# Optimization experiments

Hardware: AMD Instinct MI355X
Metric: run time of the kernel (lower is better)

The kernel has to match this reference:

```python
import jax, jax.numpy as jnp
import numpy as np

B, F = 32, 8192
GRAVITY = 9.81007
GYRO_COV = 0.0032 ** 2   # per-axis gyroscope noise covariance
ACC_COV = 0.08 ** 2      # per-axis accelerometer noise covariance


def _skew(v):
    # v: (..., 3) -> (..., 3, 3) skew-symmetric (hat) matrix
    x, y, z = v[..., 0], v[..., 1], v[..., 2]
    o = jnp.zeros_like(x)
    return jnp.stack([
        jnp.stack([o, -z, y], -1),
        jnp.stack([z, o, -x], -1),
        jnp.stack([-y, x, o], -1)], -2)


def _qmul(a, b):
    # Hamilton product, xyzw convention (pypose layout): a (x) b
    ax, ay, az, aw = a[..., 0], a[..., 1], a[..., 2], a[..., 3]
    bx, by, bz, bw = b[..., 0], b[..., 1], b[..., 2], b[..., 3]
    return jnp.stack([
        aw * bx + ax * bw + ay * bz - az * by,
        aw * by - ax * bz + ay * bw + az * bx,
        aw * bz + ax * by - ay * bx + az * bw,
        aw * bw - ax * bx - ay * by - az * bz], -1)


def _so3_exp_quat(phi):
    # so3 exponential map -> unit quaternion (xyzw), numerically safe near 0
    th2 = jnp.sum(phi * phi, -1, keepdims=True)
    small = th2 < 1e-8
    th = jnp.sqrt(jnp.where(small, 1.0, th2))
    s = jnp.where(small, 0.5 - th2 / 48.0, jnp.sin(0.5 * th) / th)
    w = jnp.where(small, 1.0 - th2 / 8.0, jnp.cos(0.5 * th))
    return jnp.concatenate([phi * s, w], -1)


def _quat_to_mat(q):
    # unit quaternion (xyzw) -> rotation matrix (..., 3, 3)
    x, y, z, w = q[..., 0], q[..., 1], q[..., 2], q[..., 3]
    r0 = jnp.stack([1 - 2 * (y * y + z * z), 2 * (x * y - z * w), 2 * (x * z + y * w)], -1)
    r1 = jnp.stack([2 * (x * y + z * w), 1 - 2 * (x * x + z * z), 2 * (y * z - x * w)], -1)
    r2 = jnp.stack([2 * (x * z - y * w), 2 * (y * z + x * w), 1 - 2 * (x * x + y * y)], -1)
    return jnp.stack([r0, r1, r2], -2)


def _so3_Jr(phi):
    # Right Jacobian of SO3: Jr = I - c1*K + c2*K^2, safe near 0
    th2 = jnp.sum(phi * phi, -1)[..., None, None]
    small = th2 < 1e-8
    th2s = jnp.where(small, 1.0, th2)
    th = jnp.sqrt(th2s)
    c1 = jnp.where(small, 0.5 - th2 / 24.0, (1.0 - jnp.cos(th)) / th2s)
    c2 = jnp.where(small, 1.0 / 6.0 - th2 / 120.0, (th - jnp.sin(th)) / (th2s * th))
    K = _skew(phi)
    I = jnp.eye(3, dtype=phi.dtype)
    return I - c1 * K + c2 * (K @ K)


def setup_inputs() -> dict:
    key = jax.random.key(0)
    k1, k2, k3 = jax.random.split(key, 3)
    dt = jax.random.uniform(k1, (B, F, 1), dtype=jnp.float32) * 0.004 + 0.001
    gyro = jax.random.normal(k2, (B, F, 3), dtype=jnp.float32)
    acc = jax.random.normal(k3, (B, F, 3), dtype=jnp.float32)
    pos0 = jnp.zeros((B, 3), dtype=jnp.float32)
    vel0 = jnp.zeros((B, 3), dtype=jnp.float32)
    return {"dt": dt, "gyro": gyro, "acc": acc, "pos0": pos0, "vel0": vel0}


def _preintegrate(dt, gyro, acc, pos0, vel0):
    dtype = acc.dtype
    g = jnp.array([0.0, 0.0, GRAVITY], dtype=dtype)
    I3 = jnp.eye(3, dtype=dtype)

    # --- rotation integration: dR_{k+1} = dR_k Exp(w_k dt_k) ---
    w = gyro * dt                                             # (B,F,3)
    dq = _so3_exp_quat(w)                                     # (B,F,4) per-step increments
    incre_q = jax.lax.associative_scan(_qmul, dq, axis=1)     # cumprod q0 (x) ... (x) qk
    R_incl = _quat_to_mat(incre_q)                            # (B,F,3,3) inclusive DeltaR_{ik+1}
    R_pre = jnp.concatenate(
        [jnp.broadcast_to(I3, (R_incl.shape[0], 1, 3, 3)), R_incl[:, :-1]], axis=1)  # DeltaR_{ik}

    # gravity removed in body frame: a_k = acc_k - R_k^{-1} g  (R^{-1} g = R^T g)
    a = acc - jnp.einsum('bfji,j->bfi', R_incl, g)            # (B,F,3)

    # --- velocity / position integration ---
    dv_step = jnp.einsum('bfij,bfj->bfi', R_pre, a) * dt      # DeltaR_{ik} a_k dt
    dvel = jnp.cumsum(dv_step, axis=1)                        # Delta v
    vel = vel0[:, None, :] + dvel
    dvel_prev = jnp.concatenate([jnp.zeros_like(dvel[:, :1]), dvel[:, :-1]], axis=1)
    dpos = jnp.cumsum(dvel_prev * dt + 0.5 * dv_step * dt, axis=1)
    pos = pos0[:, None, :] + dpos

    # --- covariance propagation: C' = A C A^T + Bg Cg Bg^T + Ba Ca Ba^T ---
    Bn, Fn = dt.shape[0], dt.shape[1]
    dRT = jnp.swapaxes(_quat_to_mat(dq), -1, -2)              # Exp(w dt)^T
    Ra = jnp.einsum('bfij,bfjk->bfik', R_pre, _skew(a))       # DeltaR (a^)
    dt1 = dt[..., None]                                       # (B,F,1,1)

    A = jnp.zeros((Bn, Fn, 9, 9), dtype=dtype)
    A = A.at[..., 0:3, 0:3].set(dRT)
    A = A.at[..., 3:6, 0:3].set(-Ra * dt1)
    A = A.at[..., 6:9, 0:3].set(-0.5 * Ra * dt1 * dt1)
    A = A.at[..., 3:6, 3:6].set(I3)
    A = A.at[..., 6:9, 6:9].set(I3)
    A = A.at[..., 6:9, 3:6].set(I3 * dt1)

    qg = jnp.full((3,), GYRO_COV, dtype=dtype)
    qa = jnp.full((3,), ACC_COV, dtype=dtype)
    Bg = _so3_Jr(w) * dt1                                     # (B,F,3,3)
    Bv = R_pre * dt1
    Bp = 0.5 * R_pre * dt1 * dt1
    Ngg = jnp.einsum('bfik,k,bfjk->bfij', Bg, qg, Bg)
    Nvv = jnp.einsum('bfik,k,bfjk->bfij', Bv, qa, Bv)
    Nvp = jnp.einsum('bfik,k,bfjk->bfij', Bv, qa, Bp)
    Npp = jnp.einsum('bfik,k,bfjk->bfij', Bp, qa, Bp)
    N = jnp.zeros((Bn, Fn, 9, 9), dtype=dtype)
    N = N.at[..., 0:3, 0:3].set(Ngg)
    N = N.at[..., 3:6, 3:6].set(Nvv)
    N = N.at[..., 3:6, 6:9].set(Nvp)
    N = N.at[..., 6:9, 3:6].set(jnp.swapaxes(Nvp, -1, -2))
    N = N.at[..., 6:9, 6:9].set(Npp)

    def step(C, AN):
        Ak, Nk = AN
        C = jnp.einsum('bij,bjk,blk->bil', Ak, C, Ak) + Nk
        return C, None

    C0 = jnp.zeros((Bn, 9, 9), dtype=dtype)
    cov, _ = jax.lax.scan(step, C0, (jnp.moveaxis(A, 1, 0), jnp.moveaxis(N, 1, 0)))

    # init rot is identity -> output rot equals the incremental cumprod
    return incre_q, vel, pos, cov


def reference(dt, gyro, acc, pos0, vel0):
    return _preintegrate(dt, gyro, acc, pos0, vel0)
```

## Files before the change

kernel.cpp:

```cpp
#include <hip/hip_runtime.h>


#define BB 32
#define FF 8192
#define NCH 128
#define SLOT 61
#define GRAV 9.81007f
#define GCOV (0.0032f*0.0032f)
#define ACOV (0.08f*0.08f)

#define COV_OFF  0
#define VPRE_OFF 249856
#define QTOT_OFF 282624
#define QPRE_OFF 299008
#define VP_OFF   315392

struct Quat { float x, y, z, w; };

__device__ __forceinline__ Quat qmul(const Quat a, const Quat b) {
    Quat r;
    r.x = a.w*b.x + a.x*b.w + a.y*b.z - a.z*b.y;
    r.y = a.w*b.y - a.x*b.z + a.y*b.w + a.z*b.x;
    r.z = a.w*b.z + a.x*b.y - a.y*b.x + a.z*b.w;
    r.w = a.w*b.w - a.x*b.x - a.y*b.y - a.z*b.z;
    return r;
}

__device__ __forceinline__ Quat qshfl_up(const Quat a, int s) {
    Quat r;
    r.x=__shfl_up(a.x,s); r.y=__shfl_up(a.y,s);
    r.z=__shfl_up(a.z,s); r.w=__shfl_up(a.w,s);
    return r;
}

__device__ __forceinline__ Quat qexp3(float px, float py, float pz) {
    float th2 = px*px + py*py + pz*pz;
    float s, w;
    if (th2 < 1e-8f) {
        s = 0.5f - th2 * (1.0f/48.0f);
        w = 1.0f - th2 * 0.125f;
    } else {
        float th = sqrtf(th2);
        s = sinf(0.5f*th) / th;
        w = cosf(0.5f*th);
    }
    Quat q; q.x=px*s; q.y=py*s; q.z=pz*s; q.w=w; return q;
}

__device__ __forceinline__ void quat2mat(const Quat q, float* R) {
    float x=q.x, y=q.y, z=q.z, w=q.w;
    R[0]=1.0f-2.0f*(y*y+z*z); R[1]=2.0f*(x*y-z*w);       R[2]=2.0f*(x*z+y*w);
    R[3]=2.0f*(x*y+z*w);      R[4]=1.0f-2.0f*(x*x+z*z);  R[5]=2.0f*(y*z-x*w);
    R[6]=2.0f*(x*z-y*w);      R[7]=2.0f*(y*z+x*w);       R[8]=1.0f-2.0f*(x*x+y*y);
}

__device__ __forceinline__ void mm_nn(const float* A, const float* B, float* C) {
#pragma unroll
    for (int i=0;i<3;i++)
#pragma unroll
    for (int j=0;j<3;j++)
        C[3*i+j] = A[3*i+0]*B[0+j] + A[3*i+1]*B[3+j] + A[3*i+2]*B[6+j];
}

__device__ __forceinline__ void mm_nt(const float* A, const float* B, float* C) {
#pragma unroll
    for (int i=0;i<3;i++)
#pragma unroll
    for (int j=0;j<3;j++)
        C[3*i+j] = A[3*i+0]*B[3*j+0] + A[3*i+1]*B[3*j+1] + A[3*i+2]*B[3*j+2];
}

__device__ __forceinline__ void mm_tn(const float* A, const float* B, float* C) {
#pragma unroll
    for (int i=0;i<3;i++)
#pragma unroll
    for (int j=0;j<3;j++)
        C[3*i+j] = A[0+i]*B[0+j] + A[3+i]*B[3+j] + A[6+i]*B[6+j];
}

__device__ __forceinline__ void mm_nt_sym(const float* A, const float* B, float* O6) {
    O6[0]=A[0]*B[0]+A[1]*B[1]+A[2]*B[2];
    O6[1]=A[0]*B[3]+A[1]*B[4]+A[2]*B[5];
    O6[2]=A[0]*B[6]+A[1]*B[7]+A[2]*B[8];
    O6[3]=A[3]*B[3]+A[4]*B[4]+A[5]*B[5];
    O6[4]=A[3]*B[6]+A[4]*B[7]+A[5]*B[8];
    O6[5]=A[6]*B[6]+A[7]*B[7]+A[8]*B[8];
}

__device__ __forceinline__ void mm_nn_sym(const float* A, const float* B, float* O6) {
    O6[0]=A[0]*B[0]+A[1]*B[3]+A[2]*B[6];
    O6[1]=A[0]*B[1]+A[1]*B[4]+A[2]*B[7];
    O6[2]=A[0]*B[2]+A[1]*B[5]+A[2]*B[8];
    O6[3]=A[3]*B[1]+A[4]*B[4]+A[5]*B[7];
    O6[4]=A[3]*B[2]+A[4]*B[5]+A[5]*B[8];
    O6[5]=A[6]*B[2]+A[7]*B[5]+A[8]*B[8];
}

__device__ __forceinline__ void expand_sym(const float* t, float* M) {
    M[0]=t[0]; M[1]=t[1]; M[2]=t[2];
    M[3]=t[1]; M[4]=t[3]; M[5]=t[4];
    M[6]=t[2]; M[7]=t[4]; M[8]=t[5];
}

__device__ __forceinline__ void m_skew(const float* M, float v0, float v1, float v2, float* C) {
#pragma unroll
    for (int i=0;i<3;i++) {
        C[3*i+0] = M[3*i+1]*v2 - M[3*i+2]*v1;
        C[3*i+1] = M[3*i+2]*v0 - M[3*i+0]*v2;
        C[3*i+2] = M[3*i+0]*v1 - M[3*i+1]*v0;
    }
}

__device__ __forceinline__ void skew_m(float w0, float w1, float w2, const float* M, float* C) {
#pragma unroll
    for (int j=0;j<3;j++) {
        C[0+j] = -w2*M[3+j] + w1*M[6+j];
        C[3+j] =  w2*M[0+j] - w0*M[6+j];
        C[6+j] = -w1*M[0+j] + w0*M[3+j];
    }
}

__global__ __launch_bounds__(256) void k_chunktot(
    const float* __restrict__ dt, const float* __restrict__ gyro,
    float* __restrict__ qtot, float* __restrict__ outq)
{
    const int bid=blockIdx.x, b=bid>>5, wg=bid&31;
    const int tid=threadIdx.x, lane=tid&63, wid=tid>>6;
    const int c=wg*4+wid;
    const long k=(long)b*FF+(long)c*64+lane;
    float d=dt[k];
    Quat inc=qexp3(gyro[3*k+0]*d, gyro[3*k+1]*d, gyro[3*k+2]*d);
#pragma unroll
    for (int s=1;s<64;s<<=1) {
        Quat p=qshfl_up(inc,s);
        if (lane>=s) inc=qmul(p,inc);
    }
    { float4 o; o.x=inc.x; o.y=inc.y; o.z=inc.z; o.w=inc.w;
      reinterpret_cast<float4*>(outq)[k]=o; }
    if (lane==63) {
        float4 o; o.x=inc.x; o.y=inc.y; o.z=inc.z; o.w=inc.w;
        reinterpret_cast<float4*>(qtot)[b*NCH+c]=o;
    }
}

__global__ __launch_bounds__(128) void k_qpre(
    const float* __restrict__ qtot, float* __restrict__ qpre)
{
    const int b=blockIdx.x, c=threadIdx.x, lane=c&63, w=c>>6;
    __shared__ float4 w0t;
    __shared__ float4 all[NCH];
    float4 t=reinterpret_cast<const float4*>(qtot)[b*NCH+c];
    Quat inc; inc.x=t.x; inc.y=t.y; inc.z=t.z; inc.w=t.w;
#pragma unroll
    for (int s=1;s<64;s<<=1) {
        Quat p=qshfl_up(inc,s);
        if (lane>=s) inc=qmul(p,inc);
    }
    if (w==0 && lane==63) { float4 o; o.x=inc.x;o.y=inc.y;o.z=inc.z;o.w=inc.w; w0t=o; }
    __syncthreads();
    if (w==1) { Quat p; p.x=w0t.x;p.y=w0t.y;p.z=w0t.z;p.w=w0t.w; inc=qmul(p,inc); }
    { float4 o; o.x=inc.x;o.y=inc.y;o.z=inc.z;o.w=inc.w; all[c]=o; }
    __syncthreads();
    float4 pre;
    if (c==0) { pre.x=0.f;pre.y=0.f;pre.z=0.f;pre.w=1.f; }
    else pre=all[c-1];
    reinterpret_cast<float4*>(qpre)[b*NCH+c]=pre;
}

#define RSTR 66
__global__ __launch_bounds__(256) void k_main(
    const float* __restrict__ dt, const float* __restrict__ gyro,
    const float* __restrict__ acc, const float* __restrict__ qpre_g,
    float* __restrict__ outq, float* __restrict__ cov, float* __restrict__ vp_g,
    float* __restrict__ outv, float* __restrict__ outp)
{
    __shared__ float red[4][23][RSTR];
    const int bid=blockIdx.x, b=bid>>5, wg=bid&31;
    const int tid=threadIdx.x, lane=tid&63, wid=tid>>6;
    const int c=wg*4+wid;
    const long k=(long)b*FF+(long)c*64+lane;

    const float d=dt[k];
    const float wx=gyro[3*k+0]*d, wy=gyro[3*k+1]*d, wz=gyro[3*k+2]*d;

    Quat qloc;
    { float4 t=reinterpret_cast<const float4*>(outq)[k];
      qloc.x=t.x; qloc.y=t.y; qloc.z=t.z; qloc.w=t.w; }
    float4 tp=reinterpret_cast<const float4*>(qpre_g)[b*NCH+c];
    Quat qpre; qpre.x=tp.x; qpre.y=tp.y; qpre.z=tp.z; qpre.w=tp.w;
    Quat qi=qmul(qpre,qloc);
    { float4 o; o.x=qi.x;o.y=qi.y;o.z=qi.z;o.w=qi.w;
      reinterpret_cast<float4*>(outq)[k]=o; }

    Quat ql1=qshfl_up(qloc,1);
    if (lane==0) { ql1.x=0.f; ql1.y=0.f; ql1.z=0.f; ql1.w=1.f; }
    Quat cq; cq.x=-ql1.x; cq.y=-ql1.y; cq.z=-ql1.z; cq.w=ql1.w;
    Quat dqq=qmul(cq,qloc);

    float a0=acc[3*k+0]-GRAV*2.0f*(qi.x*qi.z-qi.y*qi.w);
    float a1=acc[3*k+1]-GRAV*2.0f*(qi.y*qi.z+qi.x*qi.w);
    float a2=acc[3*k+2]-GRAV*(1.0f-2.0f*(qi.x*qi.x+qi.y*qi.y));

    float Rl[9]; quat2mat(ql1,Rl);
    float b0=Rl[0]*a0+Rl[1]*a1+Rl[2]*a2;
    float b1=Rl[3]*a0+Rl[4]*a1+Rl[5]*a2;
    float b2=Rl[6]*a0+Rl[7]*a1+Rl[8]*a2;
    float m0=d*b0, m1=d*b1, m2=d*b2;

    float td=d, M0=m0, M1=m1, M2=m2;
#pragma unroll
    for (int s=1;s<64;s<<=1) {
        float p3=__shfl_up(td,s), p0=__shfl_up(M0,s), p1=__shfl_up(M1,s), p2=__shfl_up(M2,s);
        if (lane>=s) { td+=p3; M0+=p0; M1+=p1; M2+=p2; }
    }
    float Dtot=__shfl(td,63);
    float tau = Dtot - td;
    float cn = 0.5f*d + tau;
    float n0=cn*m0, n1=cn*m1, n2=cn*m2;
    float N0=n0, N1=n1, N2=n2;
#pragma unroll
    for (int s=1;s<64;s<<=1) {
        float p0=__shfl_up(N0,s),p1=__shfl_up(N1,s),p2=__shfl_up(N2,s);
        if (lane>=s){ N0+=p0; N1+=p1; N2+=p2; }
    }
    float u0=(M0-0.5f*m0)*d, u1=(M1-0.5f*m1)*d, u2=(M2-0.5f*m2)*d;
    float U0=u0, U1=u1, U2=u2;
#pragma unroll
    for (int s=1;s<64;s<<=1) {
        float p0=__shfl_up(U0,s),p1=__shfl_up(U1,s),p2=__shfl_up(U2,s);
        if (lane>=s){ U0+=p0; U1+=p1; U2+=p2; }
    }
    float Mt0=__shfl(M0,63), Mt1=__shfl(M1,63), Mt2=__shfl(M2,63);
    float Nt0=__shfl(N0,63), Nt1=__shfl(N1,63), Nt2=__shfl(N2,63);
    float mp0=Mt0-M0, mp1=Mt1-M1, mp2=Mt2-M2;
    float np0=Nt0-N0, np1=Nt1-N1, np2=Nt2-N2;

    float Rp9[9]; quat2mat(qpre,Rp9);
    float pv0=Rp9[0]*M0+Rp9[1]*M1+Rp9[2]*M2;
    float pv1=Rp9[3]*M0+Rp9[4]*M1+Rp9[5]*M2;
    float pv2=Rp9[6]*M0+Rp9[7]*M1+Rp9[8]*M2;
    float pp0=Rp9[0]*U0+Rp9[1]*U1+Rp9[2]*U2;
    float pp1=Rp9[3]*U0+Rp9[4]*U1+Rp9[5]*U2;
    float pp2=Rp9[6]*U0+Rp9[7]*U1+Rp9[8]*U2;
    outv[3*k+0]=pv0; outv[3*k+1]=pv1; outv[3*k+2]=pv2;
    outp[3*k+0]=pp0; outp[3*k+1]=pp1; outp[3*k+2]=pp2;

    const long wsbase=((long)b*NCH+c)*SLOT;
    if (lane==63) {
        float* vp=vp_g+(long)(b*NCH+c)*8;
        vp[0]=pv0; vp[1]=pv1; vp[2]=pv2;
        vp[3]=pp0; vp[4]=pp1; vp[5]=pp2;
        vp[6]=td;
        cov[wsbase+45]=qloc.x; cov[wsbase+46]=qloc.y; cov[wsbase+47]=qloc.z; cov[wsbase+48]=qloc.w;
        cov[wsbase+49]=qpre.x; cov[wsbase+50]=qpre.y; cov[wsbase+51]=qpre.z; cov[wsbase+52]=qpre.w;
        cov[wsbase+53]=M0; cov[wsbase+54]=M1; cov[wsbase+55]=M2;
        cov[wsbase+56]=N0; cov[wsbase+57]=N1; cov[wsbase+58]=N2;
        cov[wsbase+59]=td;
    }

    float th2 = wx*wx + wy*wy + wz*wz;
    float c1, c2;
    if (th2 < 1e-8f) { c1 = 0.5f - th2*(1.0f/24.0f); c2 = (1.0f/6.0f) - th2*(1.0f/120.0f); }
    else {
        float s2q = dqq.x*dqq.x + dqq.y*dqq.y + dqq.z*dqq.z;
        c1 = 2.0f*s2q/th2;
        float th = sqrtf(th2);
        float snt = 2.0f*sqrtf(s2q)*dqq.w;
        c2 = (th - snt)/(th2*th);
    }
    float J[9];
    {
        float dg = 1.0f - c2*th2;
        J[0]=dg + c2*wx*wx;      J[1]= c1*wz + c2*wx*wy;  J[2]=-c1*wy + c2*wx*wz;
        J[3]=-c1*wz + c2*wx*wy;  J[4]=dg + c2*wy*wy;      J[5]= c1*wx + c2*wy*wz;
        J[6]= c1*wy + c2*wx*wz;  J[7]=-c1*wx + c2*wy*wz;  J[8]=dg + c2*wz*wz;
    }
    float Rj[9]; quat2mat(qloc,Rj);
    float H[9]; mm_nn(Rj,J,H);
    const float gs = GCOV*d*d;
    float Gp[9];
    Gp[0]=gs*(H[0]*H[0]+H[1]*H[1]+H[2]*H[2]);
    Gp[1]=gs*(H[0]*H[3]+H[1]*H[4]+H[2]*H[5]);
    Gp[2]=gs*(H[0]*H[6]+H[1]*H[7]+H[2]*H[8]);
    Gp[4]=gs*(H[3]*H[3]+H[4]*H[4]+H[5]*H[5]);
    Gp[5]=gs*(H[3]*H[6]+H[4]*H[7]+H[5]*H[8]);
    Gp[8]=gs*(H[6]*H[6]+H[7]*H[7]+H[8]*H[8]);
    Gp[3]=Gp[1]; Gp[6]=Gp[2]; Gp[7]=Gp[5];

    const float av  = ACOV*d*d;
    const float bv  = 0.5f*ACOV*d*d*d;
    const float cv  = 0.25f*ACOV*d*d*d*d;
    const float vpd = av*tau + bv;
    const float ppd = av*tau*tau + 2.0f*bv*tau + cv;

    float Crv[9], Crp[9], Cvv[9], Cvp[9], Cpp[9];
    m_skew(Gp, mp0,mp1,mp2, Crv);
    m_skew(Gp, np0,np1,np2, Crp);
    skew_m(-mp0,-mp1,-mp2, Crv, Cvv);
    skew_m(-mp0,-mp1,-mp2, Crp, Cvp);
    skew_m(-np0,-np1,-np2, Crp, Cpp);

    float S45[45];
#pragma unroll
    for (int i=0;i<9;i++){ S45[i]=Crv[i]; S45[9+i]=Crp[i]; S45[18+i]=Cvp[i]; }
    S45[18]+=vpd; S45[22]+=vpd; S45[26]+=vpd;
    S45[27]=Gp[0];  S45[28]=Gp[1];  S45[29]=Gp[2];  S45[30]=Gp[4];  S45[31]=Gp[5];  S45[32]=Gp[8];
    S45[33]=Cvv[0]+av; S45[34]=Cvv[1]; S45[35]=Cvv[2]; S45[36]=Cvv[4]+av; S45[37]=Cvv[5]; S45[38]=Cvv[8]+av;
    S45[39]=Cpp[0]+ppd; S45[40]=Cpp[1]; S45[41]=Cpp[2]; S45[42]=Cpp[4]+ppd; S45[43]=Cpp[5]; S45[44]=Cpp[8]+ppd;

#pragma unroll
    for (int e=0;e<23;e++) red[wid][e][lane] = S45[e];
    __syncthreads();
    float r1 = 0.f;
    if (lane < 23) {
        const float* row = &red[wid][lane][0];
        float ax=0.f, ay=0.f;
#pragma unroll
        for (int i=0;i<32;i++) {
            float2 v = reinterpret_cast<const float2*>(row)[i];
            ax += v.x; ay += v.y;
        }
        r1 = ax + ay;
    }
    __syncthreads();
#pragma unroll
    for (int e=0;e<22;e++) red[wid][e][lane] = S45[23+e];
    __syncthreads();
    float r2 = 0.f;
    if (lane < 22) {
        const float* row = &red[wid][lane][0];
        float ax=0.f, ay=0.f;
#pragma unroll
        for (int i=0;i<32;i++) {
            float2 v = reinterpret_cast<const float2*>(row)[i];
            ax += v.x; ay += v.y;
        }
        r2 = ax + ay;
    }
    if (lane < 23) cov[wsbase+lane] = r1;
    if (lane < 22) cov[wsbase+23+lane] = r2;
}

__global__ __launch_bounds__(128) void k_vpscan(
    const float* __restrict__ vp_g, float* __restrict__ vpre)
{
    const int b=blockIdx.x, c=threadIdx.x, lane=c&63, w=c>>6;
    __shared__ float w0t[3];
    __shared__ float all3[NCH][3];
    const float* vp=vp_g+(long)(b*NCH+c)*8;
    float Lv0=vp[0],Lv1=vp[1],Lv2=vp[2],Sw0=vp[3],Sw1=vp[4],Sw2=vp[5],Td=vp[6];

    float i0=Lv0,i1=Lv1,i2=Lv2;
#pragma unroll
    for (int s=1;s<64;s<<=1) {
        float p0=__shfl_up(i0,s),p1=__shfl_up(i1,s),p2=__shfl_up(i2,s);
        if (lane>=s){ i0+=p0; i1+=p1; i2+=p2; }
    }
    if (w==0 && lane==63){ w0t[0]=i0; w0t[1]=i1; w0t[2]=i2; }
    __syncthreads();
    if (w==1){ i0+=w0t[0]; i1+=w0t[1]; i2+=w0t[2]; }
    all3[c][0]=i0; all3[c][1]=i1; all3[c][2]=i2;
    __syncthreads();
    float V0=(c==0)?0.f:all3[c-1][0];
    float V1=(c==0)?0.f:all3[c-1][1];
    float V2=(c==0)?0.f:all3[c-1][2];
    __syncthreads();

    float u0=V0*Td+Sw0, u1=V1*Td+Sw1, u2=V2*Td+Sw2;
    i0=u0; i1=u1; i2=u2;
#pragma unroll
    for (int s=1;s<64;s<<=1) {
        float p0=__shfl_up(i0,s),p1=__shfl_up(i1,s),p2=__shfl_up(i2,s);
        if (lane>=s){ i0+=p0; i1+=p1; i2+=p2; }
    }
    if (w==0 && lane==63){ w0t[0]=i0; w0t[1]=i1; w0t[2]=i2; }
    __syncthreads();
    if (w==1){ i0+=w0t[0]; i1+=w0t[1]; i2+=w0t[2]; }
    all3[c][0]=i0; all3[c][1]=i1; all3[c][2]=i2;
    __syncthreads();
    float P0=(c==0)?0.f:all3[c-1][0];
    float P1=(c==0)?0.f:all3[c-1][1];
    float P2=(c==0)?0.f:all3[c-1][2];

    float* o=vpre+(long)(b*NCH+c)*8;
    o[0]=V0; o[1]=V1; o[2]=V2; o[3]=P0; o[4]=P1; o[5]=P2;
}

__device__ __forceinline__ void congr45(const float* Phi, const float* S, float* O)
{
    const float* D=Phi; const float* P=Phi+9; const float* Q=Phi+18; const float T=Phi[27];
    const float* Arv=S+0; const float* Arp=S+9; const float* Avp=S+18;
    float Arr[9], Avv[9], App[9];
    expand_sym(S+27,Arr); expand_sym(S+33,Avv); expand_sym(S+39,App);

    float M1[9], M2[9], M3[9], t1[9], t6[6];
    mm_nn(D,Arr,M1); mm_nn(D,Arv,M2); mm_nn(D,Arp,M3);
    mm_nt_sym(M1, D, O+27);
    mm_nt(M1, P, t1);
#pragma unroll
    for (int i=0;i<9;i++) O[0+i] = t1[i] + M2[i];
    mm_nt(M1, Q, t1);
#pragma unroll
    for (int i=0;i<9;i++) O[9+i] = t1[i] + T*M2[i] + M3[i];

    float W1[9], W2[9], W3[9];
    mm_nn(P, Arr, W1);
#pragma unroll
    for (int i=0;i<3;i++)
#pragma unroll
    for (int j=0;j<3;j++) W1[3*i+j] += Arv[3*j+i];
    mm_nn(P, Arv, W2);
#pragma unroll
    for (int i=0;i<9;i++) W2[i] += Avv[i];
    mm_nn(P, Arp, W3);
#pragma unroll
    for (int i=0;i<9;i++) W3[i] += Avp[i];
    mm_nt_sym(W1, P, t6);
    O[33+0]=t6[0]+W2[0]; O[33+1]=t6[1]+W2[1]; O[33+2]=t6[2]+W2[2];
    O[33+3]=t6[3]+W2[4]; O[33+4]=t6[4]+W2[5]; O[33+5]=t6[5]+W2[8];
    mm_nt(W1, Q, t1);
#pragma unroll
    for (int i=0;i<9;i++) O[18+i] = t1[i] + T*W2[i] + W3[i];

    float U1[9], U2[9], U3[9];
    mm_nn(Q, Arr, U1);
#pragma unroll
    for (int i=0;i<3;i++)
#pragma unroll
    for (int j=0;j<3;j++) U1[3*i+j] += T*Arv[3*j+i] + Arp[3*j+i];
    mm_nn(Q, Arv, U2);
#pragma unroll
    for (int i=0;i<3;i++)
#pragma unroll
    for (int j=0;j<3;j++) U2[3*i+j] += T*Avv[3*i+j] + Avp[3*j+i];
    mm_nn(Q, Arp, U3);
#pragma unroll
    for (int i=0;i<9;i++) U3[i] += T*Avp[i] + App[i];
    mm_nt_sym(U1, Q, t6);
    O[39+0]=t6[0]+T*U2[0]+U3[0]; O[39+1]=t6[1]+T*U2[1]+U3[1]; O[39+2]=t6[2]+T*U2[2]+U3[2];
    O[39+3]=t6[3]+T*U2[4]+U3[4]; O[39+4]=t6[4]+T*U2[5]+U3[5]; O[39+5]=t6[5]+T*U2[8]+U3[8];
}

__global__ __launch_bounds__(256) void k_merged(
    const float* __restrict__ dt, const float* __restrict__ pos0,
    const float* __restrict__ vel0, const float* __restrict__ vpre,
    const float* __restrict__ cov,
    float* __restrict__ outv, float* __restrict__ outp, float* __restrict__ outc)
{
    __shared__ float stg[NCH*SLOT];
    __shared__ float sc[NCH][13];
    const int bid=blockIdx.x;
    const int tid=threadIdx.x, lane=tid&63, wid=tid>>6;

    if (bid < BB) {
        const int b = bid;
        for (int idx=tid; idx<NCH*SLOT; idx+=256) stg[idx] = cov[(long)b*NCH*SLOT + idx];
        __syncthreads();

        if (tid < NCH) {
            const float* g = &stg[tid*SLOT];
            sc[tid][0]=g[45]; sc[tid][1]=g[46]; sc[tid][2]=g[47]; sc[tid][3]=g[48];
            sc[tid][4]=g[53]; sc[tid][5]=g[54]; sc[tid][6]=g[55];
            sc[tid][7]=g[56]; sc[tid][8]=g[57]; sc[tid][9]=g[58];
            sc[tid][10]=g[59];
        }
        __syncthreads();

        for (int s=1;s<NCH;s<<=1) {
            bool own = tid < NCH;
            bool act = own && (tid+s) < NCH;
            Quat qb, qa; float Mb[3],Nb[3],Tb=0.f, Ma[3],Na[3],Ta=0.f;
            if (own) {
                qb.x=sc[tid][0]; qb.y=sc[tid][1]; qb.z=sc[tid][2]; qb.w=sc[tid][3];
                Mb[0]=sc[tid][4]; Mb[1]=sc[tid][5]; Mb[2]=sc[tid][6];
                Nb[0]=sc[tid][7]; Nb[1]=sc[tid][8]; Nb[2]=sc[tid][9];
                Tb=sc[tid][10];
            }
            if (act) {
                qa.x=sc[tid+s][0]; qa.y=sc[tid+s][1]; qa.z=sc[tid+s][2]; qa.w=sc[tid+s][3];
                Ma[0]=sc[tid+s][4]; Ma[1]=sc[tid+s][5]; Ma[2]=sc[tid+s][6];
                Na[0]=sc[tid+s][7]; Na[1]=sc[tid+s][8]; Na[2]=sc[tid+s][9];
                Ta=sc[tid+s][10];
            }
            __syncthreads();
            if (act) {
                Quat qc=qmul(qb,qa);
                float Rb[9]; quat2mat(qb,Rb);
                float Mc0=Mb[0]+Rb[0]*Ma[0]+Rb[1]*Ma[1]+Rb[2]*Ma[2];
                float Mc1=Mb[1]+Rb[3]*Ma[0]+Rb[4]*Ma[1]+Rb[5]*Ma[2];
                float Mc2=Mb[2]+Rb[6]*Ma[0]+Rb[7]*Ma[1]+Rb[8]*Ma[2];
                float Nc0=Nb[0]+Rb[0]*Na[0]+Rb[1]*Na[1]+Rb[2]*Na[2]+Ta*Mb[0];
                float Nc1=Nb[1]+Rb[3]*Na[0]+Rb[4]*Na[1]+Rb[5]*Na[2]+Ta*Mb[1];
                float Nc2=Nb[2]+Rb[6]*Na[0]+Rb[7]*Na[1]+Rb[8]*Na[2]+Ta*Mb[2];
                sc[tid][0]=qc.x; sc[tid][1]=qc.y; sc[tid][2]=qc.z; sc[tid][3]=qc.w;
                sc[tid][4]=Mc0; sc[tid][5]=Mc1; sc[tid][6]=Mc2;
                sc[tid][7]=Nc0; sc[tid][8]=Nc1; sc[tid][9]=Nc2;
                sc[tid][10]=Ta+Tb;
            }
            __syncthreads();
        }

        if (tid < NCH) {
            const float* g = &stg[tid*SLOT];
            Quat qt; qt.x=g[45]; qt.y=g[46]; qt.z=g[47]; qt.w=g[48];
            Quat qp; qp.x=g[49]; qp.y=g[50]; qp.z=g[51]; qp.w=g[52];

            float Phi[28];
            if (tid < NCH-1) {
                Quat qs; qs.x=sc[tid+1][0]; qs.y=sc[tid+1][1]; qs.z=sc[tid+1][2]; qs.w=sc[tid+1][3];
                float Ms0=sc[tid+1][4], Ms1=sc[tid+1][5], Ms2=sc[tid+1][6];
                float Ns0=sc[tid+1][7], Ns1=sc[tid+1][8], Ns2=sc[tid+1][9];
                float Ts=sc[tid+1][10];
                float Rs[9]; quat2mat(qs,Rs);
                Phi[0]=Rs[0]; Phi[1]=Rs[3]; Phi[2]=Rs[6];
                Phi[3]=Rs[1]; Phi[4]=Rs[4]; Phi[5]=Rs[7];
                Phi[6]=Rs[2]; Phi[7]=Rs[5]; Phi[8]=Rs[8];
                Quat qp1=qmul(qp,qt);
                float Rp1[9]; quat2mat(qp1,Rp1);
                float Pc[9]; m_skew(Rp1, -Ms0,-Ms1,-Ms2, Pc);
                float Qc[9]; m_skew(Rp1, -Ns0,-Ns1,-Ns2, Qc);
#pragma unroll
                for (int i=0;i<9;i++){ Phi[9+i]=Pc[i]; Phi[18+i]=Qc[i]; }
                Phi[27]=Ts;
            } else {
#pragma unroll
                for (int i=0;i<9;i++){ Phi[i]=(i%4==0)?1.f:0.f; Phi[9+i]=0.f; Phi[18+i]=0.f; }
                Phi[27]=0.f;
            }

            float Rt[9]; quat2mat(qt,Rt);
            float Rp[9]; quat2mat(qp,Rp);
            float S[45];
            {
                float Crv[9],Crp[9],Cvp9[9], e9[9], t9[9], o9[9], o6[6];
#pragma unroll
                for (int i=0;i<9;i++){ Crv[i]=g[i]; Crp[i]=g[9+i]; Cvp9[i]=g[18+i]; }
                mm_tn(Rt, Crv, t9); mm_nt(t9, Rp, o9);
#pragma unroll
                for (int i=0;i<9;i++) S[i]=o9[i];
                mm_tn(Rt, Crp, t9); mm_nt(t9, Rp, o9);
#pragma unroll
                for (int i=0;i<9;i++) S[9+i]=o9[i];
                mm_nn(Rp, Cvp9, t9); mm_nt(t9, Rp, o9);
#pragma unroll
                for (int i=0;i<9;i++) S[18+i]=o9[i];
                expand_sym(g+27, e9); mm_tn(Rt, e9, t9); mm_nn_sym(t9, Rt, o6);
#pragma unroll
                for (int i=0;i<6;i++) S[27+i]=o6[i];
                expand_sym(g+33, e9); mm_nn(Rp, e9, t9); mm_nt_sym(t9, Rp, o6);
#pragma unroll
                for (int i=0;i<6;i++) S[33+i]=o6[i];
                expand_sym(g+39, e9); mm_nn(Rp, e9, t9); mm_nt_sym(t9, Rp, o6);
#pragma unroll
                for (int i=0;i<6;i++) S[39+i]=o6[i];
            }
            float O[45];
            congr45(Phi, S, O);
            float* w = &stg[tid*SLOT];
#pragma unroll
            for (int i=0;i<45;i++) w[i] = O[i];
        }
        __syncthreads();

        for (int s=64;s>0;s>>=1) {
            if (tid < s) {
#pragma unroll
                for (int i=0;i<45;i++) stg[tid*SLOT+i] += stg[(tid+s)*SLOT+i];
            }
            __syncthreads();
        }

        if (tid < 81) {
            int i = tid/9, j = tid%9;
            int bi = i/3, ii = i%3, bj = j/3, jj = j%3;
            int lo = (ii<jj)?ii:jj, hi = (ii<jj)?jj:ii;
            int tix = (lo==0)?hi:((lo==1)?(2+hi):5);
            const float* S0 = &stg[0];
            float v;
            if      (bi==0 && bj==0) v = S0[27 + tix];
            else if (bi==0 && bj==1) v = S0[0  + 3*ii + jj];
            else if (bi==0 && bj==2) v = S0[9  + 3*ii + jj];
            else if (bi==1 && bj==0) v = S0[0  + 3*jj + ii];
            else if (bi==1 && bj==1) v = S0[33 + tix];
            else if (bi==1 && bj==2) v = S0[18 + 3*ii + jj];
            else if (bi==2 && bj==0) v = S0[9  + 3*jj + ii];
            else if (bi==2 && bj==1) v = S0[18 + 3*jj + ii];
            else                     v = S0[39 + tix];
            outc[(long)b*81 + tid] = v;
        }
        return;
    }

    const int ebid = bid - BB;
    const int b = ebid>>5, wg = ebid&31;
    const int c = wg*4+wid;
    const long k = (long)b*FF+(long)c*64+lane;

    float td = dt[k];
#pragma unroll
    for (int s=1;s<64;s<<=1) {
        float p=__shfl_up(td,s);
        if (lane>=s) td+=p;
    }

    const float* vr=vpre+(long)(b*NCH+c)*8;
    float V0=vr[0],V1=vr[1],V2=vr[2],P0=vr[3],P1=vr[4],P2=vr[5];
    float v0x=vel0[3*b+0], v0y=vel0[3*b+1], v0z=vel0[3*b+2];
    float p0x=pos0[3*b+0], p0y=pos0[3*b+1], p0z=pos0[3*b+2];

    float pv0=outv[3*k+0], pv1=outv[3*k+1], pv2=outv[3*k+2];
    float pp0=outp[3*k+0], pp1=outp[3*k+1], pp2=outp[3*k+2];

    outv[3*k+0]=v0x+V0+pv0;
    outv[3*k+1]=v0y+V1+pv1;
    outv[3*k+2]=v0z+V2+pv2;
    outp[3*k+0]=p0x+P0+V0*td+pp0;
    outp[3*k+1]=p0y+P1+V1*td+pp1;
    outp[3*k+2]=p0z+P2+V2*td+pp2;
}

extern "C" void kernel_launch(void* const* d_in, const int* in_sizes, int n_in,
                              void* d_out, int out_size, void* d_ws, size_t ws_size,
                              hipStream_t stream)
{
    const float* dt   = (const float*)d_in[0];
    const float* gyro = (const float*)d_in[1];
    const float* acc  = (const float*)d_in[2];
    const float* pos0 = (const float*)d_in[3];
    const float* vel0 = (const float*)d_in[4];

    float* out  = (float*)d_out;
    float* outq = out;
    float* outv = out  + (long)BB*FF*4;
    float* outp = outv + (long)BB*FF*3;
    float* outc = outp + (long)BB*FF*3;

    float* ws   = (float*)d_ws;
    float* cov  = ws + COV_OFF;
    float* vpre = ws + VPRE_OFF;
    float* qtot = ws + QTOT_OFF;
    float* qpre = ws + QPRE_OFF;
    float* vp   = ws + VP_OFF;

    hipLaunchKernelGGL(k_chunktot, dim3(BB*32),    dim3(256), 0, stream, dt, gyro, qtot, outq);
    hipLaunchKernelGGL(k_qpre,     dim3(BB),       dim3(128), 0, stream, qtot, qpre);
    hipLaunchKernelGGL(k_main,     dim3(BB*32),    dim3(256), 0, stream, dt, gyro, acc, qpre, outq, cov, vp, outv, outp);
    hipLaunchKernelGGL(k_vpscan,   dim3(BB),       dim3(128), 0, stream, vp, vpre);
    hipLaunchKernelGGL(k_merged,   dim3(BB*32+BB), dim3(256), 0, stream, dt, pos0, vel0, vpre, cov, outv, outp, outc);
}
```

Baseline: 39.64 us.

## Replace shared-memory scan and tree reduction with wavefront shuffles in combine block

The per-batch combine block now runs the 128-chunk prefix scan of (quaternion, M, N, T) inside two wavefronts using shuffle-down, handing wave 1's total to wave 0 through a small shared buffer. The 45-element covariance tree reduction becomes a butterfly shuffle-xor reduction per wave, with the two wave partials summed at output. The staging slot is padded from 61 to 64 floats so the global-to-LDS copy can use aligned float4 loads, and the buffer offsets shift to match. The aim is to remove the many block-wide barriers and LDS round trips on the serial tail of the kernel, at the cost of a larger intermediate buffer and heavy shuffle traffic for the 45-float reduction.

New measurement: 36.54 us. -7.8%, faster.

```diff
diff --git a/kernel.cpp b/kernel.cpp
--- a/kernel.cpp
+++ b/kernel.cpp
@@ -4,16 +4,16 @@
 #define BB 32
 #define FF 8192
 #define NCH 128
-#define SLOT 61
+#define SLOT 64
 #define GRAV 9.81007f
 #define GCOV (0.0032f*0.0032f)
 #define ACOV (0.08f*0.08f)
 
 #define COV_OFF  0
-#define VPRE_OFF 249856
-#define QTOT_OFF 282624
-#define QPRE_OFF 299008
-#define VP_OFF   315392
+#define VPRE_OFF 262144
+#define QTOT_OFF 294912
+#define QPRE_OFF 311296
+#define VP_OFF   327680
 
 struct Quat { float x, y, z, w; };
 
@@ -448,59 +448,92 @@
     float* __restrict__ outv, float* __restrict__ outp, float* __restrict__ outc)
 {
     __shared__ float stg[NCH*SLOT];
-    __shared__ float sc[NCH][13];
+    __shared__ float sc[NCH][12];
+    __shared__ float hand[12];
+    __shared__ float wsum[2][45];
     const int bid=blockIdx.x;
     const int tid=threadIdx.x, lane=tid&63, wid=tid>>6;
 
     if (bid < BB) {
         const int b = bid;
-        for (int idx=tid; idx<NCH*SLOT; idx+=256) stg[idx] = cov[(long)b*NCH*SLOT + idx];
+        const float4* src=reinterpret_cast<const float4*>(cov + (long)b*NCH*SLOT);
+        float4* dst=reinterpret_cast<float4*>(stg);
+#pragma unroll
+        for (int j=0;j<8;j++) dst[j*256+tid]=src[j*256+tid];
         __syncthreads();
 
-        if (tid < NCH) {
-            const float* g = &stg[tid*SLOT];
-            sc[tid][0]=g[45]; sc[tid][1]=g[46]; sc[tid][2]=g[47]; sc[tid][3]=g[48];
-            sc[tid][4]=g[53]; sc[tid][5]=g[54]; sc[tid][6]=g[55];
-            sc[tid][7]=g[56]; sc[tid][8]=g[57]; sc[tid][9]=g[58];
-            sc[tid][10]=g[59];
+        const bool own = tid < NCH;
+
+        float q0,q1,q2,q3, Mv0,Mv1,Mv2, Nv0,Nv1,Nv2, Tv;
+        if (own) {
+            const float* g=&stg[tid*SLOT];
+            q0=g[45]; q1=g[46]; q2=g[47]; q3=g[48];
+            Mv0=g[53]; Mv1=g[54]; Mv2=g[55];
+            Nv0=g[56]; Nv1=g[57]; Nv2=g[58];
+            Tv=g[59];
+        } else { q0=q1=q2=0.f; q3=1.f; Mv0=Mv1=Mv2=Nv0=Nv1=Nv2=0.f; Tv=0.f; }
+
+        if (own) {
+#pragma unroll
+            for (int s=1;s<64;s<<=1) {
+                float a0=__shfl_down(q0,s), a1=__shfl_down(q1,s), a2=__shfl_down(q2,s), a3=__shfl_down(q3,s);
+                float am0=__shfl_down(Mv0,s), am1=__shfl_down(Mv1,s), am2=__shfl_down(Mv2,s);
+                float an0=__shfl_down(Nv0,s), an1=__shfl_down(Nv1,s), an2=__shfl_down(Nv2,s);
+                float aT=__shfl_down(Tv,s);
+                if (lane+s < 64) {
+                    Quat qb; qb.x=q0; qb.y=q1; qb.z=q2; qb.w=q3;
+                    Quat qa; qa.x=a0; qa.y=a1; qa.z=a2; qa.w=a3;
+                    Quat qc=qmul(qb,qa);
+                    float Rb[9]; quat2mat(qb,Rb);
+                    float Mc0=Mv0+Rb[0]*am0+Rb[1]*am1+Rb[2]*am2;
+                    float Mc1=Mv1+Rb[3]*am0+Rb[4]*am1+Rb[5]*am2;
+                    float Mc2=Mv2+Rb[6]*am0+Rb[7]*am1+Rb[8]*am2;
+                    float Nc0=Nv0+Rb[0]*an0+Rb[1]*an1+Rb[2]*an2+aT*Mv0;
+                    float Nc1=Nv1+Rb[3]*an0+Rb[4]*an1+Rb[5]*an2+aT*Mv1;
+                    float Nc2=Nv2+Rb[6]*an0+Rb[7]*an1+Rb[8]*an2+aT*Mv2;
+                    q0=qc.x; q1=qc.y; q2=qc.z; q3=qc.w;
+                    Mv0=Mc0; Mv1=Mc1; Mv2=Mc2;
+                    Nv0=Nc0; Nv1=Nc1; Nv2=Nc2;
+                    Tv+=aT;
+                }
+            }
+            if (wid==1 && lane==0) {
+                hand[0]=q0; hand[1]=q1; hand[2]=q2; hand[3]=q3;
+                hand[4]=Mv0; hand[5]=Mv1; hand[6]=Mv2;
+                hand[7]=Nv0; hand[8]=Nv1; hand[9]=Nv2;
+                hand[10]=Tv;
+            }
         }
         __syncthreads();
-
-        for (int s=1;s<NCH;s<<=1) {
-            bool own = tid < NCH;
-            bool act = own && (tid+s) < NCH;
-            Quat qb, qa; float Mb[3],Nb[3],Tb=0.f, Ma[3],Na[3],Ta=0.f;
-            if (own) {
-                qb.x=sc[tid][0]; qb.y=sc[tid][1]; qb.z=sc[tid][2]; qb.w=sc[tid][3];
-                Mb[0]=sc[tid][4]; Mb[1]=sc[tid][5]; Mb[2]=sc[tid][6];
-                Nb[0]=sc[tid][7]; Nb[1]=sc[tid][8]; Nb[2]=sc[tid][9];
-                Tb=sc[tid][10];
-            }
-            if (act) {
-                qa.x=sc[tid+s][0]; qa.y=sc[tid+s][1]; qa.z=sc[tid+s][2]; qa.w=sc[tid+s][3];
-                Ma[0]=sc[tid+s][4]; Ma[1]=sc[tid+s][5]; Ma[2]=sc[tid+s][6];
-                Na[0]=sc[tid+s][7]; Na[1]=sc[tid+s][8]; Na[2]=sc[tid+s][9];
-                Ta=sc[tid+s][10];
-            }
-            __syncthreads();
-            if (act) {
-                Quat qc=qmul(qb,qa);
-                float Rb[9]; quat2mat(qb,Rb);
-                float Mc0=Mb[0]+Rb[0]*Ma[0]+Rb[1]*Ma[1]+Rb[2]*Ma[2];
-                float Mc1=Mb[1]+Rb[3]*Ma[0]+Rb[4]*Ma[1]+Rb[5]*Ma[2];
-                float Mc2=Mb[2]+Rb[6]*Ma[0]+Rb[7]*Ma[1]+Rb[8]*Ma[2];
-                float Nc0=Nb[0]+Rb[0]*Na[0]+Rb[1]*Na[1]+Rb[2]*Na[2]+Ta*Mb[0];
-                float Nc1=Nb[1]+Rb[3]*Na[0]+Rb[4]*Na[1]+Rb[5]*Na[2]+Ta*Mb[1];
-                float Nc2=Nb[2]+Rb[6]*Na[0]+Rb[7]*Na[1]+Rb[8]*Na[2]+Ta*Mb[2];
-                sc[tid][0]=qc.x; sc[tid][1]=qc.y; sc[tid][2]=qc.z; sc[tid][3]=qc.w;
-                sc[tid][4]=Mc0; sc[tid][5]=Mc1; sc[tid][6]=Mc2;
-                sc[tid][7]=Nc0; sc[tid][8]=Nc1; sc[tid][9]=Nc2;
-                sc[tid][10]=Ta+Tb;
-            }
-            __syncthreads();
+        if (own && wid==0) {
+            Quat qb; qb.x=q0; qb.y=q1; qb.z=q2; qb.w=q3;
+            Quat qa; qa.x=hand[0]; qa.y=hand[1]; qa.z=hand[2]; qa.w=hand[3];
+            float am0=hand[4],am1=hand[5],am2=hand[6];
+            float an0=hand[7],an1=hand[8],an2=hand[9];
+            float aT=hand[10];
+            Quat qc=qmul(qb,qa);
+            float Rb[9]; quat2mat(qb,Rb);
+            float Mc0=Mv0+Rb[0]*am0+Rb[1]*am1+Rb[2]*am2;
+            float Mc1=Mv1+Rb[3]*am0+Rb[4]*am1+Rb[5]*am2;
+            float Mc2=Mv2+Rb[6]*am0+Rb[7]*am1+Rb[8]*am2;
+            float Nc0=Nv0+Rb[0]*an0+Rb[1]*an1+Rb[2]*an2+aT*Mv0;
+            float Nc1=Nv1+Rb[3]*an0+Rb[4]*an1+Rb[5]*an2+aT*Mv1;
+            float Nc2=Nv2+Rb[6]*an0+Rb[7]*an1+Rb[8]*an2+aT*Mv2;
+            q0=qc.x; q1=qc.y; q2=qc.z; q3=qc.w;
+            Mv0=Mc0; Mv1=Mc1; Mv2=Mc2;
+            Nv0=Nc0; Nv1=Nc1; Nv2=Nc2;
+            Tv+=aT;
         }
-
-        if (tid < NCH) {
+        if (own) {
+            sc[tid][0]=q0; sc[tid][1]=q1; sc[tid][2]=q2; sc[tid][3]=q3;
+            sc[tid][4]=Mv0; sc[tid][5]=Mv1; sc[tid][6]=Mv2;
+            sc[tid][7]=Nv0; sc[tid][8]=Nv1; sc[tid][9]=Nv2;
+            sc[tid][10]=Tv;
+        }
+        __syncthreads();
+
+        float O[45];
+        if (own) {
             const float* g = &stg[tid*SLOT];
             Quat qt; qt.x=g[45]; qt.y=g[46]; qt.z=g[47]; qt.w=g[48];
             Quat qp; qp.x=g[49]; qp.y=g[50]; qp.z=g[51]; qp.w=g[52];
@@ -554,39 +587,36 @@
 #pragma unroll
                 for (int i=0;i<6;i++) S[39+i]=o6[i];
             }
-            float O[45];
             congr45(Phi, S, O);
-            float* w = &stg[tid*SLOT];
-#pragma unroll
-            for (int i=0;i<45;i++) w[i] = O[i];
+
+#pragma unroll
+            for (int m=1;m<64;m<<=1) {
+#pragma unroll
+                for (int i=0;i<45;i++) O[i] += __shfl_xor(O[i], m);
+            }
+            if (lane==0) {
+#pragma unroll
+                for (int i=0;i<45;i++) wsum[wid][i] = O[i];
+            }
         }
         __syncthreads();
-
-        for (int s=64;s>0;s>>=1) {
-            if (tid < s) {
-#pragma unroll
-                for (int i=0;i<45;i++) stg[tid*SLOT+i] += stg[(tid+s)*SLOT+i];
-            }
-            __syncthreads();
-        }
 
         if (tid < 81) {
             int i = tid/9, j = tid%9;
             int bi = i/3, ii = i%3, bj = j/3, jj = j%3;
             int lo = (ii<jj)?ii:jj, hi = (ii<jj)?jj:ii;
             int tix = (lo==0)?hi:((lo==1)?(2+hi):5);
-            const float* S0 = &stg[0];
-            float v;
-            if      (bi==0 && bj==0) v = S0[27 + tix];
-            else if (bi==0 && bj==1) v = S0[0  + 3*ii + jj];
-            else if (bi==0 && bj==2) v = S0[9  + 3*ii + jj];
-            else if (bi==1 && bj==0) v = S0[0  + 3*jj + ii];
-            else if (bi==1 && bj==1) v = S0[33 + tix];
-            else if (bi==1 && bj==2) v = S0[18 + 3*ii + jj];
-            else if (bi==2 && bj==0) v = S0[9  + 3*jj + ii];
-            else if (bi==2 && bj==1) v = S0[18 + 3*jj + ii];
-            else                     v = S0[39 + tix];
-            outc[(long)b*81 + tid] = v;
+            int x;
+            if      (bi==0 && bj==0) x = 27 + tix;
+            else if (bi==0 && bj==1) x = 0  + 3*ii + jj;
+            else if (bi==0 && bj==2) x = 9  + 3*ii + jj;
+            else if (bi==1 && bj==0) x = 0  + 3*jj + ii;
+            else if (bi==1 && bj==1) x = 33 + tix;
+            else if (bi==1 && bj==2) x = 18 + 3*ii + jj;
+            else if (bi==2 && bj==0) x = 9  + 3*jj + ii;
+            else if (bi==2 && bj==1) x = 18 + 3*jj + ii;
+            else                     x = 39 + tix;
+            outc[(long)b*81 + tid] = wsum[0][x] + wsum[1][x];
         }
         return;
     }
```
